# Kernel tuning notes

Measured on AMD Instinct MI355X. Metric: run time of the kernel, lower is better.

## Reference

```python
import jax, jax.numpy as jnp
import numpy as np

D_MODEL = 1024
NUM_HEADS = 16
HEAD_DIM = D_MODEL // NUM_HEADS
SEQ_LEN = 2048
THETA = 10000.0


def setup_inputs() -> dict:
    key = jax.random.key(0)
    ks = jax.random.split(key, 9)
    s = 1.0 / np.sqrt(D_MODEL)
    inp = {
        "x": jax.random.normal(ks[0], (2, SEQ_LEN, D_MODEL), dtype=jnp.float32),
        "Wq": jax.random.uniform(ks[1], (D_MODEL, D_MODEL), jnp.float32, -s, s),
        "bq": jax.random.uniform(ks[2], (D_MODEL,), jnp.float32, -s, s),
        "Wk": jax.random.uniform(ks[3], (D_MODEL, D_MODEL), jnp.float32, -s, s),
        "bk": jax.random.uniform(ks[4], (D_MODEL,), jnp.float32, -s, s),
        "Wv": jax.random.uniform(ks[5], (D_MODEL, D_MODEL), jnp.float32, -s, s),
        "bv": jax.random.uniform(ks[6], (D_MODEL,), jnp.float32, -s, s),
        "Wo": jax.random.uniform(ks[7], (D_MODEL, D_MODEL), jnp.float32, -s, s),
        "bo": jax.random.uniform(ks[8], (D_MODEL,), jnp.float32, -s, s),
    }
    return inp


def _rope_cos_sin(seq_len, dim, theta):
    inv_freq = 1.0 / theta ** (jnp.arange(0, dim, 2, dtype=jnp.float32) / dim)  # [dim/2]
    t = jnp.arange(seq_len, dtype=jnp.float32)
    freqs = jnp.outer(t, inv_freq)  # [S, dim/2]
    return jnp.cos(freqs), jnp.sin(freqs)


def _apply_rope(x, cos, sin):
    # x: [B, H, S, head_dim]; interleaved complex pairs (even, odd)
    x2 = x.reshape(*x.shape[:-1], -1, 2)  # [B,H,S,hd/2,2]
    xe, xo = x2[..., 0], x2[..., 1]
    c = cos[None, None, :, :]
    s = sin[None, None, :, :]
    oe = xe * c - xo * s
    oo = xe * s + xo * c
    return jnp.stack([oe, oo], axis=-1).reshape(x.shape)


def reference(x, Wq, bq, Wk, bk, Wv, bv, Wo, bo):
    B, S, D = x.shape
    H, hd = NUM_HEADS, HEAD_DIM
    q = x @ Wq.T + bq
    k = x @ Wk.T + bk
    v = x @ Wv.T + bv
    # [B, H, S, hd]
    q = q.reshape(B, S, H, hd).transpose(0, 2, 1, 3)
    k = k.reshape(B, S, H, hd).transpose(0, 2, 1, 3)
    v = v.reshape(B, S, H, hd).transpose(0, 2, 1, 3)
    cos, sin = _rope_cos_sin(S, hd, THETA)
    q = _apply_rope(q, cos, sin)
    k = _apply_rope(k, cos, sin)
    scores = jnp.einsum("bhqd,bhkd->bhqk", q, k) / jnp.sqrt(jnp.float32(hd))
    causal = jnp.triu(jnp.ones((S, S), dtype=bool), k=1)
    scores = jnp.where(causal[None, None, :, :], -jnp.inf, scores)
    attn = jax.nn.softmax(scores, axis=-1)
    out = jnp.einsum("bhqk,bhkd->bhqd", attn, v)
    out = out.transpose(0, 2, 1, 3).reshape(B, S, D)
    return out @ Wo.T + bo
```

## Files before the change

kernel.cpp:

```cpp
#include <hip/hip_runtime.h>
#include <hip/hip_bf16.h>

#define S_LEN 2048
#define DM 1024
#define NH 16
#define HD 64
#define M_ROWS 4096
#define LOG2E 1.4426950408889634f
#define MASKVAL -1.0e4f
#define QSCALE 0.18033688011112042f

typedef __attribute__((ext_vector_type(8))) short short8;
typedef __attribute__((ext_vector_type(2))) float f32x2;
typedef __attribute__((ext_vector_type(4))) float f32x4;
typedef __attribute__((ext_vector_type(16))) float f32x16;

__device__ inline ushort f2b(float f) {
  union { float f; unsigned u; } v; v.f = f;
  unsigned r = v.u + 0x7fffu + ((v.u >> 16) & 1u);
  return (ushort)(r >> 16);
}

__device__ inline float b2f(ushort u) {
  union { unsigned u; float f; } v; v.u = ((unsigned)u) << 16; return v.f;
}

__device__ inline unsigned pk_bf16(float a, float b) {
  __hip_bfloat162 h = __float22bfloat162_rn(make_float2(a, b));
  union { __hip_bfloat162 h; unsigned u; } v; v.h = h;
  return v.u;
}

__device__ inline float fexp2(float x) { return __builtin_amdgcn_exp2f(x); }

__device__ inline void gl_lds16(const void* g, void* l) {
  __builtin_amdgcn_global_load_lds(
      (const __attribute__((address_space(1))) void*)g,
      (__attribute__((address_space(3))) void*)l, 16, 0, 0);
}

__global__ __launch_bounds__(256) void cast_rope_kernel(
    const float* __restrict__ x, const float* __restrict__ Wq, const float* __restrict__ Wk,
    const float* __restrict__ Wv, const float* __restrict__ Wo,
    ushort* __restrict__ xb, ushort* __restrict__ Wqb, ushort* __restrict__ Wkb,
    ushort* __restrict__ Wvb, ushort* __restrict__ Wob,
    float* __restrict__ ropeC, float* __restrict__ ropeS) {
  const int bid = blockIdx.x;
  if (bid >= 8192) {
    int idx = (bid - 8192) * 256 + threadIdx.x;
    int s = idx >> 5, i = idx & 31;
    float inv = exp2f(-(float)i * (13.287712379549449f / 32.0f));
    float a = (float)s * inv;
    ropeC[idx] = cosf(a);
    ropeS[idx] = sinf(a);
    return;
  }
  int i = bid * 256 + threadIdx.x;
  int r = i >> 18, off = i & 0x3FFFF;
  const float4* s;
  uint2* d;
  switch (r) {
    case 0: case 1: case 2: case 3: s = (const float4*)x + i;  d = (uint2*)xb + i;  break;
    case 4: s = (const float4*)Wq + off; d = (uint2*)Wqb + off; break;
    case 5: s = (const float4*)Wk + off; d = (uint2*)Wkb + off; break;
    case 6: s = (const float4*)Wv + off; d = (uint2*)Wvb + off; break;
    default: s = (const float4*)Wo + off; d = (uint2*)Wob + off; break;
  }
  float4 v = *s;
  uint2 o;
  o.x = pk_bf16(v.x, v.y);
  o.y = pk_bf16(v.z, v.w);
  *d = o;
}

__global__ __launch_bounds__(256) void gemm_qkv_kernel(const ushort* __restrict__ xb,
    const ushort* __restrict__ Wqb, const ushort* __restrict__ Wkb, const ushort* __restrict__ Wvb,
    const float* __restrict__ bq, const float* __restrict__ bk, const float* __restrict__ bv,
    const float* __restrict__ ropeC, const float* __restrict__ ropeS,
    ushort* __restrict__ qb, ushort* __restrict__ kb, ushort* __restrict__ vT) {
  __shared__ ushort lds[24576];
  const int lid = blockIdx.x;
  const int swz = (lid & 7) * 96 + (lid >> 3);
  const int z = swz >> 8;
  const int rem = swz & 255;
  const int m0 = (rem & 31) * 128, n0 = (rem >> 5) * 128;
  const ushort* W = (z == 0) ? Wqb : ((z == 1) ? Wkb : Wvb);
  const float* bias = (z == 0) ? bq : ((z == 1) ? bk : bv);
  const int t = threadIdx.x, lane = t & 63, wave = t >> 6;
  const int wr = (wave >> 1) * 64, wc = (wave & 1) * 64;
  const int lr = lane & 15, lg = lane >> 4;

  const int slot0 = wave * 128 + lane, slot1 = slot0 + 64;
  const int row0 = slot0 >> 2, g0 = (slot0 & 3) ^ (row0 & 3);
  const int row1 = slot1 >> 2, g1 = (slot1 & 3) ^ (row1 & 3);
  const ushort* Ap0 = &xb[(size_t)(m0 + row0) * DM + g0 * 8];
  const ushort* Ap1 = &xb[(size_t)(m0 + row1) * DM + g1 * 8];
  const ushort* Wp0 = &W[(size_t)(n0 + row0) * DM + g0 * 8];
  const ushort* Wp1 = &W[(size_t)(n0 + row1) * DM + g1 * 8];

  f32x4 acc[4][4];
#pragma unroll
  for (int a = 0; a < 4; a++)
#pragma unroll
    for (int b = 0; b < 4; b++) acc[a][b] = (f32x4){0.f, 0.f, 0.f, 0.f};

  gl_lds16(Ap0, &lds[slot0 * 8]);
  gl_lds16(Ap1, &lds[slot1 * 8]);
  gl_lds16(Wp0, &lds[12288 + slot0 * 8]);
  gl_lds16(Wp1, &lds[12288 + slot1 * 8]);
  gl_lds16(Ap0 + 32, &lds[4096 + slot0 * 8]);
  gl_lds16(Ap1 + 32, &lds[4096 + slot1 * 8]);
  gl_lds16(Wp0 + 32, &lds[16384 + slot0 * 8]);
  gl_lds16(Wp1 + 32, &lds[16384 + slot1 * 8]);
  asm volatile("s_waitcnt vmcnt(4)" ::: "memory");
  __builtin_amdgcn_s_barrier();
  __builtin_amdgcn_sched_barrier(0);

  int cur = 0;
  for (int i = 0; i < 32; i++) {
    const bool pref = (i + 2 < 32);
    if (pref) {
      const int nb = (cur >= 1) ? cur - 1 : 2;
      const int k0 = (i + 2) * 32;
      gl_lds16(Ap0 + k0, &lds[nb * 4096 + slot0 * 8]);
      gl_lds16(Ap1 + k0, &lds[nb * 4096 + slot1 * 8]);
      gl_lds16(Wp0 + k0, &lds[12288 + nb * 4096 + slot0 * 8]);
      gl_lds16(Wp1 + k0, &lds[12288 + nb * 4096 + slot1 * 8]);
    }
    const int fb = cur * 4096;
    short8 af[4], bf[4];
#pragma unroll
    for (int mt = 0; mt < 4; mt++) {
      const int row = wr + mt * 16 + lr;
      af[mt] = *(const short8*)&lds[fb + (row * 4 + (lg ^ (row & 3))) * 8];
    }
#pragma unroll
    for (int nt = 0; nt < 4; nt++) {
      const int row = wc + nt * 16 + lr;
      bf[nt] = *(const short8*)&lds[12288 + fb + (row * 4 + (lg ^ (row & 3))) * 8];
    }
#pragma unroll
    for (int mt = 0; mt < 4; mt++)
#pragma unroll
      for (int nt = 0; nt < 4; nt++)
        acc[mt][nt] = __builtin_amdgcn_mfma_f32_16x16x32_bf16(af[mt], bf[nt], acc[mt][nt], 0, 0, 0);
    if (i + 1 < 32) {
      if (pref) asm volatile("s_waitcnt vmcnt(4)" ::: "memory");
      else      asm volatile("s_waitcnt vmcnt(0)" ::: "memory");
      __builtin_amdgcn_s_barrier();
      __builtin_amdgcn_sched_barrier(0);
    }
    cur = (cur >= 2) ? 0 : cur + 1;
  }
  __syncthreads();

#pragma unroll
  for (int mt = 0; mt < 4; mt++) {
#pragma unroll
    for (int nt = 0; nt < 4; nt++) {
      const int nloc = wc + nt * 16 + lr;
      const float bn = bias[n0 + nloc];
#pragma unroll
      for (int r = 0; r < 4; r++) {
        const int mloc = wr + mt * 16 + lg * 4 + r;
        const ushort v = f2b(acc[mt][nt][r] + bn);
        if (z < 2) lds[mloc * 136 + nloc] = v;
        else       lds[nloc * 136 + mloc] = v;
      }
    }
  }
  __syncthreads();

  const int b = m0 >> 11;
  if (z < 2) {
    ushort* dst = (z == 0) ? qb : kb;
    const float qscale = (z == 0) ? QSCALE : 1.0f;
#pragma unroll
    for (int c = 0; c < 8; c++) {
      const int sloc = c * 16 + (t >> 4);
      const int nloc = (t & 15) * 8;
      short8 val = *(const short8*)&lds[sloc * 136 + nloc];
      const int s = (m0 + sloc) & (S_LEN - 1);
      const int h = (n0 + nloc) >> 6;
      const int d0 = nloc & 63;
      const float4 cv = *(const float4*)&ropeC[s * 32 + d0 / 2];
      const float4 sv = *(const float4*)&ropeS[s * 32 + d0 / 2];
      uint4 o;
      {
        float e = b2f((ushort)val[0]), od = b2f((ushort)val[1]);
        o.x = pk_bf16((e * cv.x - od * sv.x) * qscale, (e * sv.x + od * cv.x) * qscale);
      }
      {
        float e = b2f((ushort)val[2]), od = b2f((ushort)val[3]);
        o.y = pk_bf16((e * cv.y - od * sv.y) * qscale, (e * sv.y + od * cv.y) * qscale);
      }
      {
        float e = b2f((ushort)val[4]), od = b2f((ushort)val[5]);
        o.z = pk_bf16((e * cv.z - od * sv.z) * qscale, (e * sv.z + od * cv.z) * qscale);
      }
      {
        float e = b2f((ushort)val[6]), od = b2f((ushort)val[7]);
        o.w = pk_bf16((e * cv.w - od * sv.w) * qscale, (e * sv.w + od * cv.w) * qscale);
      }
      *(uint4*)&dst[(((size_t)b * NH + h) * S_LEN + s) * HD + d0] = o;
    }
  } else {
    const int sbase = m0 & (S_LEN - 1);
#pragma unroll
    for (int c = 0; c < 8; c++) {
      const int nloc = c * 16 + (t >> 4);
      const int s0 = (t & 15) * 8;
      short8 val = *(const short8*)&lds[nloc * 136 + s0];
      const int h = (n0 + nloc) >> 6;
      const int d = nloc & 63;
      *(short8*)&vT[(((size_t)b * NH + h) * HD + d) * S_LEN + sbase + s0] = val;
    }
  }
}

__global__ __launch_bounds__(256) void flash_kernel(const ushort* __restrict__ qb,
                                                    const ushort* __restrict__ kb,
                                                    const ushort* __restrict__ vT,
                                                    ushort* __restrict__ Oh,
                                                    float* __restrict__ lsum) {
  __shared__ ushort lds[24576];
  const int t = threadIdx.x, lane = t & 63, wave = t >> 6;
  const int q31 = lane & 31, h = lane >> 5;
  const int lid = blockIdx.x + 40 * blockIdx.y;
  const int swz = (lid & 7) * 160 + (lid >> 3);
  const int bh = swz / 40;
  const int cid = swz - bh * 40;
  const int g = (cid >= 24) ? 3 : (cid >= 12) ? 2 : (cid >= 4) ? 1 : 0;
  const int nc = g + 1;
  const int o = cid - 4 * ((g * (g + 1)) >> 1);
  const int qi = o / nc;
  const int c = o - qi * nc;
  const int qt = g * 4 + qi;
  const int q0 = qt * 128;
  const int ntiles = 2 * qt + 2;
  const int kstart = c * 8;
  const int kend = min(kstart + 8, ntiles);
  const int pidx = bh * 40 + cid;

  const ushort* kbh = kb + (size_t)bh * S_LEN * HD;
  const ushort* vbh = vT + (size_t)bh * HD * S_LEN;

  const int qrow = q0 + wave * 32 + q31;
  const ushort* qptr = qb + ((size_t)bh * S_LEN + qrow) * HD + h * 8;
  short8 qf[4];
#pragma unroll
  for (int s = 0; s < 4; s++) qf[s] = *(const short8*)(qptr + s * 16);

  const int slot0 = wave * 128 + lane, slot1 = slot0 + 64;
  const int row0 = slot0 >> 3, g0 = (slot0 & 7) ^ (row0 & 7);
  const int row1 = slot1 >> 3, g1 = (slot1 & 7) ^ (row1 & 7);
  const int lo0 = wave * 128 * 8, lo1 = lo0 + 64 * 8;

  int foff[4][2];
#pragma unroll
  for (int s = 0; s < 4; s++)
#pragma unroll
    for (int st = 0; st < 2; st++) {
      const int row = st * 32 + q31;
      foff[s][st] = (row * 8 + ((2 * s + h) ^ (row & 7))) * 8;
    }

  const ushort* kp0 = kbh + (size_t)(kstart * 64 + row0) * HD + g0 * 8;
  const ushort* kp1 = kbh + (size_t)(kstart * 64 + row1) * HD + g1 * 8;
  const ushort* vp0 = vbh + (size_t)row0 * S_LEN + kstart * 64 + g0 * 8;
  const ushort* vp1 = vbh + (size_t)row1 * S_LEN + kstart * 64 + g1 * 8;
  gl_lds16(kp0, &lds[lo0]);
  gl_lds16(kp1, &lds[lo1]);
  gl_lds16(vp0, &lds[12288 + lo0]);
  gl_lds16(vp1, &lds[12288 + lo1]);
  kp0 += 64 * HD; kp1 += 64 * HD; vp0 += 64; vp1 += 64;
  gl_lds16(kp0, &lds[4096 + lo0]);
  gl_lds16(kp1, &lds[4096 + lo1]);
  gl_lds16(vp0, &lds[16384 + lo0]);
  gl_lds16(vp1, &lds[16384 + lo1]);
  kp0 += 64 * HD; kp1 += 64 * HD; vp0 += 64; vp1 += 64;

  f32x16 O[2];
#pragma unroll
  for (int st = 0; st < 2; st++)
#pragma unroll
    for (int r = 0; r < 16; r++) O[st][r] = 0.f;

  f32x16 zc;
#pragma unroll
  for (int r = 0; r < 16; r++) zc[r] = 0.f;

  f32x2 lpA = (f32x2){0.f, 0.f}, lpB = (f32x2){0.f, 0.f};

  asm volatile("s_waitcnt vmcnt(4)" ::: "memory");
  __builtin_amdgcn_s_barrier();
  __builtin_amdgcn_sched_barrier(0);

  int cur = 0;
  for (int kt = kstart; kt < kend; ++kt) {
    const bool pref = (kt + 2 < kend);
    if (pref) {
      const int nb = (cur >= 1) ? cur - 1 : 2;
      const int ko = nb * 4096, vo = 12288 + nb * 4096;
      gl_lds16(kp0, &lds[ko + lo0]);
      gl_lds16(kp1, &lds[ko + lo1]);
      gl_lds16(vp0, &lds[vo + lo0]);
      gl_lds16(vp1, &lds[vo + lo1]);
      kp0 += 64 * HD; kp1 += 64 * HD; vp0 += 64; vp1 += 64;
    }
    const ushort* Kb = &lds[cur * 4096];
    const ushort* Vb = &lds[12288 + cur * 4096];

    f32x16 sc0, sc1;
    __builtin_amdgcn_s_setprio(1);
    sc0 = __builtin_amdgcn_mfma_f32_32x32x16_bf16(
        *(const short8*)&Kb[foff[0][0]], qf[0], zc, 0, 0, 0);
    sc1 = __builtin_amdgcn_mfma_f32_32x32x16_bf16(
        *(const short8*)&Kb[foff[0][1]], qf[0], zc, 0, 0, 0);
#pragma unroll
    for (int s = 1; s < 4; s++) {
      sc0 = __builtin_amdgcn_mfma_f32_32x32x16_bf16(
          *(const short8*)&Kb[foff[s][0]], qf[s], sc0, 0, 0, 0);
      sc1 = __builtin_amdgcn_mfma_f32_32x32x16_bf16(
          *(const short8*)&Kb[foff[s][1]], qf[s], sc1, 0, 0, 0);
    }
    __builtin_amdgcn_s_setprio(0);

    if (kt * 64 + 63 > q0 + wave * 32) {
#pragma unroll
      for (int r = 0; r < 16; r++) {
        const int kc0 = kt * 64 + (r & 3) + 8 * (r >> 2) + 4 * h;
        if (kc0 > qrow) sc0[r] = MASKVAL;
        if (kc0 + 32 > qrow) sc1[r] = MASKVAL;
      }
    }
#pragma unroll
    for (int r = 0; r < 16; r += 2) {
      const float a0 = fexp2(sc0[r]), a1 = fexp2(sc0[r + 1]);
      const float b0 = fexp2(sc1[r]), b1 = fexp2(sc1[r + 1]);
      sc0[r] = a0; sc0[r + 1] = a1;
      sc1[r] = b0; sc1[r + 1] = b1;
      lpA += (f32x2){a0, a1};
      lpB += (f32x2){b0, b1};
    }

    unsigned pp[8][2];
#pragma unroll
    for (int rg = 0; rg < 4; rg++) {
      pp[rg][0] = pk_bf16(sc0[4 * rg + 0], sc0[4 * rg + 1]);
      pp[rg][1] = pk_bf16(sc0[4 * rg + 2], sc0[4 * rg + 3]);
      pp[4 + rg][0] = pk_bf16(sc1[4 * rg + 0], sc1[4 * rg + 1]);
      pp[4 + rg][1] = pk_bf16(sc1[4 * rg + 2], sc1[4 * rg + 3]);
    }
    __builtin_amdgcn_s_setprio(1);
#pragma unroll
    for (int s = 0; s < 4; s++) {
      unsigned d0 = pp[2 * s][0], e0 = pp[2 * s + 1][0];
      unsigned d1 = pp[2 * s][1], e1 = pp[2 * s + 1][1];
      asm("v_permlane32_swap_b32 %0, %1" : "+v"(d0), "+v"(e0));
      asm("v_permlane32_swap_b32 %0, %1" : "+v"(d1), "+v"(e1));
      union { unsigned u[4]; short8 v; } pf;
      pf.u[0] = d0;
      pf.u[1] = d1;
      pf.u[2] = e0;
      pf.u[3] = e1;
      O[0] = __builtin_amdgcn_mfma_f32_32x32x16_bf16(
          *(const short8*)&Vb[foff[s][0]], pf.v, O[0], 0, 0, 0);
      O[1] = __builtin_amdgcn_mfma_f32_32x32x16_bf16(
          *(const short8*)&Vb[foff[s][1]], pf.v, O[1], 0, 0, 0);
    }
    __builtin_amdgcn_s_setprio(0);

    if (kt + 1 < kend) {
      if (pref) asm volatile("s_waitcnt vmcnt(4)" ::: "memory");
      else      asm volatile("s_waitcnt vmcnt(0)" ::: "memory");
      __builtin_amdgcn_s_barrier();
      __builtin_amdgcn_sched_barrier(0);
    }
    cur = (cur >= 2) ? 0 : cur + 1;
  }

  float lacc = (lpA[0] + lpA[1]) + (lpB[0] + lpB[1]);
  lacc += __shfl_xor(lacc, 32);

  ushort* obase = Oh + ((size_t)pidx * 128 + wave * 32 + q31) * HD;
#pragma unroll
  for (int st = 0; st < 2; st++)
#pragma unroll
    for (int rg = 0; rg < 4; rg++) {
      const int d0 = st * 32 + 8 * rg + 4 * h;
      uint2 w;
      w.x = pk_bf16(O[st][4 * rg + 0], O[st][4 * rg + 1]);
      w.y = pk_bf16(O[st][4 * rg + 2], O[st][4 * rg + 3]);
      *(uint2*)&obase[d0] = w;
    }
  if (h == 0) lsum[(size_t)pidx * 128 + wave * 32 + q31] = lacc;
}

__global__ __launch_bounds__(256) void combine_kernel(const ushort* __restrict__ Oh,
                                                      const float* __restrict__ lsum,
                                                      ushort* __restrict__ attn) {
  const int tid = blockIdx.x * 256 + threadIdx.x;
  const int d8 = tid & 7;
  const int q = (tid >> 3) & (S_LEN - 1);
  const int bh = tid >> 14;
  const int qt = q >> 7, row = q & 127;
  const int g = qt >> 2, nc = g + 1;
  const int base = 4 * ((g * (g + 1)) >> 1) + (qt & 3) * nc;
  const int p0 = bh * 40 + base;

  float l = 0.f;
  float acc[8];
#pragma unroll
  for (int j = 0; j < 8; j++) acc[j] = 0.f;
  for (int c = 0; c < nc; c++) {
    const size_t rowidx = (size_t)(p0 + c) * 128 + row;
    l += lsum[rowidx];
    const uint4 a = *(const uint4*)&Oh[rowidx * HD + d8 * 8];
    const unsigned au[4] = {a.x, a.y, a.z, a.w};
#pragma unroll
    for (int j = 0; j < 4; j++) {
      acc[2 * j] += b2f((ushort)(au[j] & 0xffff));
      acc[2 * j + 1] += b2f((ushort)(au[j] >> 16));
    }
  }
  const float inv = 1.f / l;
  uint4 o;
  unsigned* op = (unsigned*)&o;
#pragma unroll
  for (int j = 0; j < 4; j++) op[j] = pk_bf16(acc[2 * j] * inv, acc[2 * j + 1] * inv);
  const int b = bh >> 4, hh = bh & 15;
  *(uint4*)&attn[((size_t)b * S_LEN + q) * DM + hh * HD + d8 * 8] = o;
}

__global__ __launch_bounds__(256) void gemm_out_kernel(const ushort* __restrict__ attn,
                                                       const ushort* __restrict__ Wob,
                                                       const float* __restrict__ bo,
                                                       float* __restrict__ out) {
  __shared__ ushort lds[18432];
  const int lid = blockIdx.x;
  const int swz = (lid & 7) * 64 + (lid >> 3);
  const int m0 = (swz & 31) * 128, n0 = (swz >> 5) * 64;
  const int t = threadIdx.x, lane = t & 63, wave = t >> 6;
  const int wm = (wave >> 1) * 64, wn = (wave & 1) * 32;
  const int lr = lane & 15, lg = lane >> 4;
  const int slotA0 = wave * 128 + lane, slotA1 = slotA0 + 64;
  const int rowA0 = slotA0 >> 2, gA0 = (slotA0 & 3) ^ (rowA0 & 3);
  const int rowA1 = slotA1 >> 2, gA1 = (slotA1 & 3) ^ (rowA1 & 3);
  const int slotB = wave * 64 + lane;
  const int rowB = slotB >> 2, gB = (slotB & 3) ^ (rowB & 3);
  const ushort* Ap0 = &attn[(size_t)(m0 + rowA0) * DM + gA0 * 8];
  const ushort* Ap1 = &attn[(size_t)(m0 + rowA1) * DM + gA1 * 8];
  const ushort* Wp  = &Wob[(size_t)(n0 + rowB) * DM + gB * 8];

  f32x4 acc[4][2];
#pragma unroll
  for (int a = 0; a < 4; a++)
#pragma unroll
    for (int b = 0; b < 2; b++) acc[a][b] = (f32x4){0.f, 0.f, 0.f, 0.f};

  gl_lds16(Ap0, &lds[slotA0 * 8]);
  gl_lds16(Ap1, &lds[slotA1 * 8]);
  gl_lds16(Wp, &lds[12288 + slotB * 8]);
  gl_lds16(Ap0 + 32, &lds[4096 + slotA0 * 8]);
  gl_lds16(Ap1 + 32, &lds[4096 + slotA1 * 8]);
  gl_lds16(Wp + 32, &lds[14336 + slotB * 8]);
  asm volatile("s_waitcnt vmcnt(3)" ::: "memory");
  __builtin_amdgcn_s_barrier();
  __builtin_amdgcn_sched_barrier(0);

  int cur = 0;
  for (int i = 0; i < 32; i++) {
    const bool pref = (i + 2 < 32);
    if (pref) {
      const int nb = (cur >= 1) ? cur - 1 : 2;
      const int k0 = (i + 2) * 32;
      gl_lds16(Ap0 + k0, &lds[nb * 4096 + slotA0 * 8]);
      gl_lds16(Ap1 + k0, &lds[nb * 4096 + slotA1 * 8]);
      gl_lds16(Wp + k0, &lds[12288 + nb * 2048 + slotB * 8]);
    }
    short8 af[4], bf[2];
#pragma unroll
    for (int mt = 0; mt < 4; mt++) {
      const int row = wm + mt * 16 + lr;
      af[mt] = *(const short8*)&lds[cur * 4096 + (row * 4 + (lg ^ (row & 3))) * 8];
    }
#pragma unroll
    for (int nt = 0; nt < 2; nt++) {
      const int row = wn + nt * 16 + lr;
      bf[nt] = *(const short8*)&lds[12288 + cur * 2048 + (row * 4 + (lg ^ (row & 3))) * 8];
    }
#pragma unroll
    for (int mt = 0; mt < 4; mt++)
#pragma unroll
      for (int nt = 0; nt < 2; nt++)
        acc[mt][nt] = __builtin_amdgcn_mfma_f32_16x16x32_bf16(af[mt], bf[nt], acc[mt][nt], 0, 0, 0);
    if (i + 1 < 32) {
      if (pref) asm volatile("s_waitcnt vmcnt(3)" ::: "memory");
      else      asm volatile("s_waitcnt vmcnt(0)" ::: "memory");
      __builtin_amdgcn_s_barrier();
      __builtin_amdgcn_sched_barrier(0);
    }
    cur = (cur >= 2) ? 0 : cur + 1;
  }

#pragma unroll
  for (int mt = 0; mt < 4; mt++) {
#pragma unroll
    for (int nt = 0; nt < 2; nt++) {
      const int n = n0 + wn + nt * 16 + lr;
      const float bn = bo[n];
#pragma unroll
      for (int r = 0; r < 4; r++) {
        const int m = m0 + wm + mt * 16 + lg * 4 + r;
        out[(size_t)m * DM + n] = acc[mt][nt][r] + bn;
      }
    }
  }
}

extern "C" void kernel_launch(void* const* d_in, const int* in_sizes, int n_in,
                              void* d_out, int out_size, void* d_ws, size_t ws_size,
                              hipStream_t stream) {
  const float* x  = (const float*)d_in[0];
  const float* Wq = (const float*)d_in[1];
  const float* bq = (const float*)d_in[2];
  const float* Wk = (const float*)d_in[3];
  const float* bk = (const float*)d_in[4];
  const float* Wv = (const float*)d_in[5];
  const float* bv = (const float*)d_in[6];
  const float* Wo = (const float*)d_in[7];
  const float* bo = (const float*)d_in[8];
  float* out = (float*)d_out;

  char* ws = (char*)d_ws;
  size_t off = 0;
  auto alloc = [&](size_t bytes) { char* p = ws + off; off += (bytes + 255) & ~255ull; return p; };
  ushort* xb   = (ushort*)alloc((size_t)M_ROWS * DM * 2);
  ushort* Wqb  = (ushort*)alloc((size_t)DM * DM * 2);
  ushort* Wkb  = (ushort*)alloc((size_t)DM * DM * 2);
  ushort* Wvb  = (ushort*)alloc((size_t)DM * DM * 2);
  ushort* Wob  = (ushort*)alloc((size_t)DM * DM * 2);
  ushort* qb   = (ushort*)alloc((size_t)M_ROWS * DM * 2);
  ushort* kb   = (ushort*)alloc((size_t)M_ROWS * DM * 2);
  ushort* vTb  = (ushort*)alloc((size_t)M_ROWS * DM * 2);
  ushort* attn = (ushort*)alloc((size_t)M_ROWS * DM * 2);
  ushort* Ohb  = (ushort*)alloc((size_t)1280 * 128 * HD * 2);
  float* lsb   = (float*)alloc((size_t)1280 * 128 * 4);
  float* ropeC = (float*)alloc((size_t)S_LEN * 32 * 4);
  float* ropeS = (float*)alloc((size_t)S_LEN * 32 * 4);
  (void)ws_size; (void)in_sizes; (void)n_in; (void)out_size;

  cast_rope_kernel<<<8448, 256, 0, stream>>>(x, Wq, Wk, Wv, Wo, xb, Wqb, Wkb, Wvb, Wob,
                                             ropeC, ropeS);
  gemm_qkv_kernel<<<768, 256, 0, stream>>>(
      xb, Wqb, Wkb, Wvb, bq, bk, bv, ropeC, ropeS, qb, kb, vTb);
  flash_kernel<<<dim3(40, 32), 256, 0, stream>>>(qb, kb, vTb, Ohb, lsb);
  combine_kernel<<<2048, 256, 0, stream>>>(Ohb, lsb, attn);
  gemm_out_kernel<<<512, 256, 0, stream>>>(attn, Wob, bo, out);
}
```

Measured before the change: 193.5 us.

## Drop split-KV flash decomposition and combine kernel, use one block per query tile

Replaces the split-KV scheme (1280 blocks, each covering up to 8 key tiles, followed by a combine kernel) with 512 blocks that each process the full causal key range for one 128-row query tile. Blocks are ordered longest-first so the heavy tiles start early. Normalization now happens in-kernel and results go straight to the attention buffer, which removes the partial-output traffic and one launch. The cost is less parallelism and more load imbalance: 512 blocks with up to 32 key tiles each, against 1280 shorter blocks.

```diff
diff --git a/kernel.cpp b/kernel.cpp
--- a/kernel.cpp
+++ b/kernel.cpp
@@ -221,26 +221,18 @@
 __global__ __launch_bounds__(256) void flash_kernel(const ushort* __restrict__ qb,
                                                     const ushort* __restrict__ kb,
                                                     const ushort* __restrict__ vT,
-                                                    ushort* __restrict__ Oh,
-                                                    float* __restrict__ lsum) {
+                                                    ushort* __restrict__ attn) {
   __shared__ ushort lds[24576];
   const int t = threadIdx.x, lane = t & 63, wave = t >> 6;
   const int q31 = lane & 31, h = lane >> 5;
-  const int lid = blockIdx.x + 40 * blockIdx.y;
-  const int swz = (lid & 7) * 160 + (lid >> 3);
-  const int bh = swz / 40;
-  const int cid = swz - bh * 40;
-  const int g = (cid >= 24) ? 3 : (cid >= 12) ? 2 : (cid >= 4) ? 1 : 0;
-  const int nc = g + 1;
-  const int o = cid - 4 * ((g * (g + 1)) >> 1);
-  const int qi = o / nc;
-  const int c = o - qi * nc;
-  const int qt = g * 4 + qi;
+  const int lid = blockIdx.x;
+  const int g = lid >> 5;
+  const int qt = (g < 8) ? (15 - g) : (g - 8);
+  const int bh = lid & 31;
   const int q0 = qt * 128;
   const int ntiles = 2 * qt + 2;
-  const int kstart = c * 8;
-  const int kend = min(kstart + 8, ntiles);
-  const int pidx = bh * 40 + cid;
+  const int kstart = 0;
+  const int kend = ntiles;
 
   const ushort* kbh = kb + (size_t)bh * S_LEN * HD;
   const ushort* vbh = vT + (size_t)bh * HD * S_LEN;
@@ -265,10 +257,10 @@
       foff[s][st] = (row * 8 + ((2 * s + h) ^ (row & 7))) * 8;
     }
 
-  const ushort* kp0 = kbh + (size_t)(kstart * 64 + row0) * HD + g0 * 8;
-  const ushort* kp1 = kbh + (size_t)(kstart * 64 + row1) * HD + g1 * 8;
-  const ushort* vp0 = vbh + (size_t)row0 * S_LEN + kstart * 64 + g0 * 8;
-  const ushort* vp1 = vbh + (size_t)row1 * S_LEN + kstart * 64 + g1 * 8;
+  const ushort* kp0 = kbh + (size_t)row0 * HD + g0 * 8;
+  const ushort* kp1 = kbh + (size_t)row1 * HD + g1 * 8;
+  const ushort* vp0 = vbh + (size_t)row0 * S_LEN + g0 * 8;
+  const ushort* vp1 = vbh + (size_t)row1 * S_LEN + g1 * 8;
   gl_lds16(kp0, &lds[lo0]);
   gl_lds16(kp1, &lds[lo1]);
   gl_lds16(vp0, &lds[12288 + lo0]);
@@ -382,55 +374,21 @@
 
   float lacc = (lpA[0] + lpA[1]) + (lpB[0] + lpB[1]);
   lacc += __shfl_xor(lacc, 32);
-
-  ushort* obase = Oh + ((size_t)pidx * 128 + wave * 32 + q31) * HD;
+  const float inv = 1.f / lacc;
+
+  const int b = bh >> 4, hh = bh & 15;
+  const int q = q0 + wave * 32 + q31;
+  ushort* obase = attn + ((size_t)b * S_LEN + q) * DM + hh * HD;
 #pragma unroll
   for (int st = 0; st < 2; st++)
 #pragma unroll
     for (int rg = 0; rg < 4; rg++) {
       const int d0 = st * 32 + 8 * rg + 4 * h;
       uint2 w;
-      w.x = pk_bf16(O[st][4 * rg + 0], O[st][4 * rg + 1]);
-      w.y = pk_bf16(O[st][4 * rg + 2], O[st][4 * rg + 3]);
+      w.x = pk_bf16(O[st][4 * rg + 0] * inv, O[st][4 * rg + 1] * inv);
+      w.y = pk_bf16(O[st][4 * rg + 2] * inv, O[st][4 * rg + 3] * inv);
       *(uint2*)&obase[d0] = w;
     }
-  if (h == 0) lsum[(size_t)pidx * 128 + wave * 32 + q31] = lacc;
-}
-
-__global__ __launch_bounds__(256) void combine_kernel(const ushort* __restrict__ Oh,
-                                                      const float* __restrict__ lsum,
-                                                      ushort* __restrict__ attn) {
-  const int tid = blockIdx.x * 256 + threadIdx.x;
-  const int d8 = tid & 7;
-  const int q = (tid >> 3) & (S_LEN - 1);
-  const int bh = tid >> 14;
-  const int qt = q >> 7, row = q & 127;
-  const int g = qt >> 2, nc = g + 1;
-  const int base = 4 * ((g * (g + 1)) >> 1) + (qt & 3) * nc;
-  const int p0 = bh * 40 + base;
-
-  float l = 0.f;
-  float acc[8];
-#pragma unroll
-  for (int j = 0; j < 8; j++) acc[j] = 0.f;
-  for (int c = 0; c < nc; c++) {
-    const size_t rowidx = (size_t)(p0 + c) * 128 + row;
-    l += lsum[rowidx];
-    const uint4 a = *(const uint4*)&Oh[rowidx * HD + d8 * 8];
-    const unsigned au[4] = {a.x, a.y, a.z, a.w};
-#pragma unroll
-    for (int j = 0; j < 4; j++) {
-      acc[2 * j] += b2f((ushort)(au[j] & 0xffff));
-      acc[2 * j + 1] += b2f((ushort)(au[j] >> 16));
-    }
-  }
-  const float inv = 1.f / l;
-  uint4 o;
-  unsigned* op = (unsigned*)&o;
-#pragma unroll
-  for (int j = 0; j < 4; j++) op[j] = pk_bf16(acc[2 * j] * inv, acc[2 * j + 1] * inv);
-  const int b = bh >> 4, hh = bh & 15;
-  *(uint4*)&attn[((size_t)b * S_LEN + q) * DM + hh * HD + d8 * 8] = o;
 }
 
 __global__ __launch_bounds__(256) void gemm_out_kernel(const ushort* __restrict__ attn,
@@ -545,8 +503,6 @@
   ushort* kb   = (ushort*)alloc((size_t)M_ROWS * DM * 2);
   ushort* vTb  = (ushort*)alloc((size_t)M_ROWS * DM * 2);
   ushort* attn = (ushort*)alloc((size_t)M_ROWS * DM * 2);
-  ushort* Ohb  = (ushort*)alloc((size_t)1280 * 128 * HD * 2);
-  float* lsb   = (float*)alloc((size_t)1280 * 128 * 4);
   float* ropeC = (float*)alloc((size_t)S_LEN * 32 * 4);
   float* ropeS = (float*)alloc((size_t)S_LEN * 32 * 4);
   (void)ws_size; (void)in_sizes; (void)n_in; (void)out_size;
@@ -555,7 +511,6 @@
                                              ropeC, ropeS);
   gemm_qkv_kernel<<<768, 256, 0, stream>>>(
       xb, Wqb, Wkb, Wvb, bq, bk, bv, ropeC, ropeS, qb, kb, vTb);
-  flash_kernel<<<dim3(40, 32), 256, 0, stream>>>(qb, kb, vTb, Ohb, lsb);
-  combine_kernel<<<2048, 256, 0, stream>>>(Ohb, lsb, attn);
+  flash_kernel<<<512, 256, 0, stream>>>(qb, kb, vTb, attn);
   gemm_out_kernel<<<512, 256, 0, stream>>>(attn, Wob, bo, out);
 }
```

Measured after the change: 188.0 us. 2.8% less time.
